# Kernel tuning notes

Hardware: AMD Instinct MI355X
Metric: run time of the kernel (lower is better)

Reference implementation:

```python
import jax, jax.numpy as jnp
import numpy as np

B, NQ, NKV = 16, 4096, 77
QUERY_DIM, CONTEXT_DIM = 320, 768
HEADS, DIM_HEAD = 8, 64
INNER = HEADS * DIM_HEAD
SCALE = DIM_HEAD ** (-0.5)
MAX_NEG = -jnp.finfo(jnp.float32).max / 2


def setup_inputs() -> dict:
    key = jax.random.key(0)
    ks = jax.random.split(key, 8)
    x = jax.random.normal(ks[0], (B, NQ, QUERY_DIM), dtype=jnp.float32)
    context = jax.random.normal(ks[1], (B, NKV, CONTEXT_DIM), dtype=jnp.float32)
    mask = jax.random.randint(ks[2], (B, 1, 1, NKV), 0, 2).astype(bool)
    s = 0.02
    Wq = jax.random.normal(ks[3], (QUERY_DIM, INNER), dtype=jnp.float32) * s
    Wk = jax.random.normal(ks[4], (CONTEXT_DIM, INNER), dtype=jnp.float32) * s
    Wv = jax.random.normal(ks[5], (CONTEXT_DIM, INNER), dtype=jnp.float32) * s
    Wo = jax.random.normal(ks[6], (INNER, QUERY_DIM), dtype=jnp.float32) * s
    bo = jnp.zeros((QUERY_DIM,), dtype=jnp.float32)
    return {"x": x, "context": context, "mask": mask,
            "Wq": Wq, "Wk": Wk, "Wv": Wv, "Wo": Wo, "bo": bo}


def reference(x, context, mask, Wq, Wk, Wv, Wo, bo):
    # projections (bias-free Linears)
    q = (x @ Wq).reshape(B, NQ, HEADS, DIM_HEAD)        # b q h d
    k = (context @ Wk).reshape(B, NKV, HEADS, DIM_HEAD)  # b k h d
    v = (context @ Wv).reshape(B, NKV, HEADS, DIM_HEAD)  # b k h d
    # additive mask bias: 0 where mask, -finfo.max/2 where ~mask (matches masked_fill_)
    bias = jnp.where(mask, jnp.float32(0), MAX_NEG)      # broadcast to b h q k
    sim = jnp.einsum('bqhd,bkhd->bhqk', q, k) * SCALE + bias
    attn = jax.nn.softmax(sim, axis=-1)
    out = jnp.einsum('bhqk,bkhd->bqhd', attn, v).reshape(B, NQ, INNER)
    return out @ Wo + bo  # dropout p=0 -> identity
```

## Files before the change

kernel.cpp:

```cpp
#include <hip/hip_runtime.h>

typedef unsigned short ushort_t;
typedef __attribute__((ext_vector_type(8))) short bf16x8;
typedef __attribute__((ext_vector_type(4))) float f32x4;

#define B_SZ   16
#define NQ     4096
#define NKV    77
#define QDIM   320
#define CDIM   768
#define HEADS  8
#define DHEAD  64
#define INNER  512
#define M_ROWS (B_SZ * NQ)
#define VT_STR 104

__device__ __forceinline__ ushort_t f2bf(float f) {
  unsigned u = __builtin_bit_cast(unsigned, f);
  u = (u + 0x7fffu + ((u >> 16) & 1u)) >> 16;
  return (ushort_t)u;
}

__device__ __forceinline__ void async16(const ushort_t* g, ushort_t* l) {
  __builtin_amdgcn_global_load_lds(
      (const __attribute__((address_space(1))) unsigned int*)g,
      (__attribute__((address_space(3))) unsigned int*)l,
      16, 0, 0);
}

#define VMCNT(N) asm volatile("s_waitcnt vmcnt(" #N ")" ::: "memory")

__global__ void mask_bias_kernel(const unsigned char* __restrict__ mraw,
                                 float* __restrict__ biasT) {
  __shared__ int s_u8, s_w4;
  if (threadIdx.x == 0) { s_u8 = 0; s_w4 = 0; }
  __syncthreads();
  const int nbytes = B_SZ * NKV;
  for (int i = threadIdx.x; i < nbytes; i += blockDim.x) {
    unsigned char v = mraw[i];
    if (v && (i & 3)) atomicOr(&s_u8, 1);
    if (v && ((i & 7) == 4)) atomicOr(&s_w4, 1);
  }
  __syncthreads();
  int mode = s_u8 ? 0 : (s_w4 ? 1 : 2);
  for (int i = threadIdx.x; i < B_SZ * 80; i += blockDim.x) {
    int b = i / 80, kv = i - b * 80;
    float bias = -2e30f;
    if (kv < NKV) {
      int idx = b * NKV + kv;
      long long m;
      if (mode == 0)      m = (long long)mraw[idx];
      else if (mode == 1) m = (long long)((const int*)mraw)[idx];
      else                m = ((const long long*)mraw)[idx];
      bias = m ? 0.0f : -1e30f;
    }
    biasT[i] = bias;
  }
}

__global__ void cast_f32_bf16(const float* __restrict__ in,
                              ushort_t* __restrict__ out, int n4) {
  int i = blockIdx.x * blockDim.x + threadIdx.x;
  int stride = gridDim.x * blockDim.x;
  const float4* in4 = (const float4*)in;
  ushort4* out4 = (ushort4*)out;
  for (; i < n4; i += stride) {
    float4 v = in4[i];
    ushort4 o;
    o.x = f2bf(v.x); o.y = f2bf(v.y); o.z = f2bf(v.z); o.w = f2bf(v.w);
    out4[i] = o;
  }
}

__global__ void tcast_f32_bf16(const float* __restrict__ in,
                               ushort_t* __restrict__ out,
                               int K, int N, int Npad, float scale) {
  int i = blockIdx.x * blockDim.x + threadIdx.x;
  int stride = gridDim.x * blockDim.x;
  int total = Npad * K;
  for (; i < total; i += stride) {
    int n = i / K, k = i - n * K;
    out[i] = (n < N) ? f2bf(in[(size_t)k * N + n] * scale) : (ushort_t)0;
  }
}

__global__ void vtrans_kernel(const ushort_t* __restrict__ kvb,
                              ushort_t* __restrict__ vt) {
  const int h = blockIdx.y, b = blockIdx.z;
  const int wid = threadIdx.x >> 6, lane = threadIdx.x & 63;
  const int d = blockIdx.x * 4 + wid;
  ushort_t* dst = vt + (size_t)(b * HEADS + h) * (64 * VT_STR) + d * VT_STR;
  for (int kv = lane; kv < VT_STR; kv += 64)
    dst[kv] = (kv < NKV)
        ? kvb[(size_t)(b * NKV + kv) * 1024 + 512 + h * 64 + d]
        : (ushort_t)0;
}

__global__ __launch_bounds__(256) void gemm_bf16(
    const ushort_t* __restrict__ A, const ushort_t* __restrict__ Bt,
    ushort_t* __restrict__ Cb,
    int K, int Astride, int Bstride, int Cstride) {
  __shared__ ushort_t As[128 * 64];
  __shared__ ushort_t Bs[128 * 64];
  const int tid = threadIdx.x;
  const int wid = tid >> 6, lane = tid & 63;
  const int wr = wid >> 1, wc = wid & 1;
  const int tileM = blockIdx.x * 128, tileN = blockIdx.y * 128;

  f32x4 acc[4][4];
#pragma unroll
  for (int m = 0; m < 4; ++m)
#pragma unroll
    for (int n = 0; n < 4; ++n) acc[m][n] = (f32x4){0.f, 0.f, 0.f, 0.f};

  const int srow = lane >> 3;
  const int scol = (lane & 7) * 8;

  for (int kt = 0; kt < K; kt += 64) {
    __syncthreads();
#pragma unroll
    for (int j = 0; j < 4; ++j) {
      int s = wid * 4 + j;
      const ushort_t* ga = A + (size_t)(tileM + s * 8 + srow) * Astride + kt + scol;
      const ushort_t* gb = Bt + (size_t)(tileN + s * 8 + srow) * Bstride + kt + scol;
      async16(ga, As + s * 512);
      async16(gb, Bs + s * 512);
    }
    __syncthreads();
#pragma unroll
    for (int kc = 0; kc < 2; ++kc) {
      bf16x8 af[4], bfr[4];
#pragma unroll
      for (int m = 0; m < 4; ++m)
        af[m] = *(const bf16x8*)&As[(wr * 64 + m * 16 + (lane & 15)) * 64 + kc * 32 + (lane >> 4) * 8];
#pragma unroll
      for (int n = 0; n < 4; ++n)
        bfr[n] = *(const bf16x8*)&Bs[(wc * 64 + n * 16 + (lane & 15)) * 64 + kc * 32 + (lane >> 4) * 8];
#pragma unroll
      for (int m = 0; m < 4; ++m)
#pragma unroll
        for (int n = 0; n < 4; ++n)
          acc[m][n] = __builtin_amdgcn_mfma_f32_16x16x32_bf16(af[m], bfr[n], acc[m][n], 0, 0, 0);
    }
  }

  const int r0 = tileM + wr * 64;
  const int c0 = tileN + wc * 64;
  const int rl2 = (lane >> 4) * 4;
  const int cl = lane & 15;
#pragma unroll
  for (int m = 0; m < 4; ++m)
#pragma unroll
    for (int n = 0; n < 4; ++n) {
      int col = c0 + n * 16 + cl;
#pragma unroll
      for (int r = 0; r < 4; ++r)
        Cb[(size_t)(r0 + m * 16 + rl2 + r) * Cstride + col] = f2bf(acc[m][n][r]);
    }
}

__global__ __launch_bounds__(512, 2) void gemm_qproj_p(
    const float* __restrict__ x, const ushort_t* __restrict__ Wt,
    ushort_t* __restrict__ qb) {
  extern __shared__ char sm[];
  const int tid = threadIdx.x, wid = tid >> 6, lane = tid & 63;
  const int rl = lane & 15, g = lane >> 4;
  const int wr = wid & 1, wc = wid >> 1;
  const size_t Mbase = (size_t)blockIdx.x * 128;

  size_t asrc[2]; unsigned adst[2];
#pragma unroll
  for (int i = 0; i < 2; ++i) {
    int c = tid + i * 512, row = c >> 3, c16 = c & 7;
    asrc[i] = (Mbase + row) * 1280 + (unsigned)((c16 * 16) ^ ((row & 7) << 4));
    adst[i] = c * 16;
  }
  size_t bsrc[4]; unsigned bdst[4];
#pragma unroll
  for (int i = 0; i < 4; ++i) {
    int c = tid + i * 512, row = c >> 2, c16 = c & 3;
    bsrc[i] = (size_t)row * 640 + (unsigned)((c16 * 16) ^ ((row & 3) << 4));
    bdst[i] = 16384 + c * 16;
  }
  const char* xB = (const char*)x;
  const char* WtB = (const char*)Wt;

  f32x4 acc[4][8];
#pragma unroll
  for (int m = 0; m < 4; ++m)
#pragma unroll
    for (int n = 0; n < 8; ++n) acc[m][n] = (f32x4){0.f, 0.f, 0.f, 0.f};

#define QSTAGE(K)                                                           \
  {                                                                         \
    char* bb = sm + (unsigned)((K) % 3) * 49152u;                           \
    _Pragma("unroll")                                                       \
    for (int i = 0; i < 2; ++i)                                             \
      async16((const ushort_t*)(xB + asrc[i] + (size_t)(K) * 128),          \
              (ushort_t*)(bb + adst[i]));                                   \
    _Pragma("unroll")                                                       \
    for (int i = 0; i < 4; ++i)                                             \
      async16((const ushort_t*)(WtB + bsrc[i] + (size_t)(K) * 64),          \
              (ushort_t*)(bb + bdst[i]));                                   \
  }

  QSTAGE(0)
  QSTAGE(1)
  for (int s = 0; s < 10; ++s) {
    if (s < 8) QSTAGE(s + 2)
    if (s < 8)       { VMCNT(12); }
    else if (s == 8) { VMCNT(6); }
    else             { VMCNT(0); }
    __builtin_amdgcn_sched_barrier(0);
    __builtin_amdgcn_s_barrier();
    __builtin_amdgcn_sched_barrier(0);

    const char* Ab = sm + (unsigned)(s % 3) * 49152u;
    const char* Bb = Ab + 16384;
    bf16x8 af[4], bfr[8];
#pragma unroll
    for (int m = 0; m < 4; ++m) {
      const int row = wr * 64 + m * 16 + rl;
      const int sw = (row & 7) << 4;
      f32x4 lo = *(const f32x4*)(Ab + row * 128 + ((g * 32) ^ sw));
      f32x4 hi = *(const f32x4*)(Ab + row * 128 + ((g * 32 + 16) ^ sw));
      unsigned w0, w1, w2, w3;
      asm("v_cvt_pk_bf16_f32 %0, %1, %2" : "=v"(w0) : "v"(lo[0]), "v"(lo[1]));
      asm("v_cvt_pk_bf16_f32 %0, %1, %2" : "=v"(w1) : "v"(lo[2]), "v"(lo[3]));
      asm("v_cvt_pk_bf16_f32 %0, %1, %2" : "=v"(w2) : "v"(hi[0]), "v"(hi[1]));
      asm("v_cvt_pk_bf16_f32 %0, %1, %2" : "=v"(w3) : "v"(hi[2]), "v"(hi[3]));
      union { unsigned u[4]; bf16x8 v; } cv;
      cv.u[0] = w0; cv.u[1] = w1; cv.u[2] = w2; cv.u[3] = w3;
      af[m] = cv.v;
    }
#pragma unroll
    for (int n = 0; n < 8; ++n) {
      const int row = wc * 128 + n * 16 + rl;
      bfr[n] = *(const bf16x8*)(Bb + row * 64 + ((g * 16) ^ ((row & 3) << 4)));
    }
#pragma unroll
    for (int m = 0; m < 4; ++m)
#pragma unroll
      for (int n = 0; n < 8; ++n)
        acc[m][n] = __builtin_amdgcn_mfma_f32_16x16x32_bf16(af[m], bfr[n], acc[m][n], 0, 0, 0);
    __builtin_amdgcn_sched_barrier(0);
    __builtin_amdgcn_s_barrier();
    __builtin_amdgcn_sched_barrier(0);
  }

  ushort_t* eb = (ushort_t*)sm;
#pragma unroll
  for (int h = 0; h < 2; ++h) {
    if (h) __syncthreads();
    if (wr == h) {
#pragma unroll
      for (int m = 0; m < 4; ++m)
#pragma unroll
        for (int n = 0; n < 8; ++n)
#pragma unroll
          for (int r = 0; r < 4; ++r)
            eb[(m * 16 + g * 4 + r) * 512 + wc * 128 + n * 16 + rl] = f2bf(acc[m][n][r]);
    }
    __syncthreads();
#pragma unroll
    for (int i = 0; i < 8; ++i) {
      int c = tid + i * 512, row = c >> 6;
      *(bf16x8*)(qb + (Mbase + h * 64 + row) * 512 + (c & 63) * 8) =
          *(const bf16x8*)(eb + c * 8);
    }
  }
}

__global__ __launch_bounds__(512, 2) void gemm_oproj_p(
    const ushort_t* __restrict__ A, const ushort_t* __restrict__ Wt,
    const float* __restrict__ bo, float* __restrict__ out) {
  extern __shared__ char sm[];
  const int tid = threadIdx.x, wid = tid >> 6, lane = tid & 63;
  const int rl = lane & 15, g = lane >> 4;
  const int wr = wid & 1, wc = wid >> 1;
  const size_t Mbase = (size_t)blockIdx.x * 128;

  size_t asrc; unsigned adst;
  {
    int c = tid, row = c >> 2, c16 = c & 3;
    asrc = (Mbase + row) * 1024 + (unsigned)((c16 * 16) ^ ((row & 3) << 4));
    adst = c * 16;
  }
  size_t bsrc[3]; unsigned bdst[3];
#pragma unroll
  for (int i = 0; i < 3; ++i) {
    int c = tid + i * 512, row = c >> 2, c16 = c & 3;
    bsrc[i] = (size_t)row * 1024 + (unsigned)((c16 * 16) ^ ((row & 3) << 4));
    bdst[i] = 8192 + c * 16;
  }
  const char* AB = (const char*)A;
  const char* WtB = (const char*)Wt;

  f32x4 acc[4][6];
#pragma unroll
  for (int m = 0; m < 4; ++m)
#pragma unroll
    for (int n = 0; n < 6; ++n) acc[m][n] = (f32x4){0.f, 0.f, 0.f, 0.f};

#define OSTAGE(K)                                                           \
  {                                                                         \
    char* bb = sm + (unsigned)((K) % 3) * 32768u;                           \
    async16((const ushort_t*)(AB + asrc + (size_t)(K) * 64),                \
            (ushort_t*)(bb + adst));                                        \
    _Pragma("unroll")                                                       \
    for (int i = 0; i < 3; ++i)                                             \
      async16((const ushort_t*)(WtB + bsrc[i] + (size_t)(K) * 64),          \
              (ushort_t*)(bb + bdst[i]));                                   \
  }

  OSTAGE(0)
  OSTAGE(1)
  for (int s = 0; s < 16; ++s) {
    if (s < 14) OSTAGE(s + 2)
    if (s < 14)       { VMCNT(8); }
    else if (s == 14) { VMCNT(4); }
    else              { VMCNT(0); }
    __builtin_amdgcn_sched_barrier(0);
    __builtin_amdgcn_s_barrier();
    __builtin_amdgcn_sched_barrier(0);

    const char* Ab = sm + (unsigned)(s % 3) * 32768u;
    const char* Bb = Ab + 8192;
    bf16x8 af[4], bfr[6];
#pragma unroll
    for (int m = 0; m < 4; ++m) {
      const int row = wr * 64 + m * 16 + rl;
      af[m] = *(const bf16x8*)(Ab + row * 64 + ((g * 16) ^ ((row & 3) << 4)));
    }
#pragma unroll
    for (int n = 0; n < 6; ++n) {
      const int row = wc * 96 + n * 16 + rl;
      bfr[n] = *(const bf16x8*)(Bb + row * 64 + ((g * 16) ^ ((row & 3) << 4)));
    }
#pragma unroll
    for (int m = 0; m < 4; ++m)
#pragma unroll
      for (int n = 0; n < 6; ++n)
        acc[m][n] = __builtin_amdgcn_mfma_f32_16x16x32_bf16(af[m], bfr[n], acc[m][n], 0, 0, 0);
    __builtin_amdgcn_sched_barrier(0);
    __builtin_amdgcn_s_barrier();
    __builtin_amdgcn_sched_barrier(0);
  }

  const size_t r0 = Mbase + wr * 64;
  const int c0 = wc * 96;
#pragma unroll
  for (int n = 0; n < 6; ++n) {
    int col = c0 + n * 16 + rl;
    if (col < QDIM) {
      float bv = bo[col];
#pragma unroll
      for (int m = 0; m < 4; ++m)
#pragma unroll
        for (int r = 0; r < 4; ++r)
          out[(r0 + m * 16 + g * 4 + r) * QDIM + col] = acc[m][n][r] + bv;
    }
  }
}

__global__ __launch_bounds__(256) void attn_kernel(
    const ushort_t* __restrict__ qb, const ushort_t* __restrict__ kvb,
    const ushort_t* __restrict__ vt, const float* __restrict__ biasT,
    ushort_t* __restrict__ ab) {
  __shared__ ushort_t Vt[64 * VT_STR];
  __shared__ ushort_t P[4 * 16 * VT_STR];
  const int qt = blockIdx.x, h = blockIdx.y, b = blockIdx.z;
  const int tid = threadIdx.x, wid = tid >> 6, lane = tid & 63;
  const int rl = lane & 15;
  const int kh = (lane >> 4) * 8;

  const ushort_t* vtg = vt + (size_t)(b * HEADS + h) * (64 * VT_STR);
  for (int i = tid; i < 832; i += 256) async16(vtg + i * 8, Vt + i * 8);
  for (int i = tid; i < 832; i += 256)
    *(bf16x8*)&P[i * 8] = (bf16x8){0, 0, 0, 0, 0, 0, 0, 0};

  bf16x8 kf[5][2];
  float bias_v[5];
#pragma unroll
  for (int nt = 0; nt < 5; ++nt) {
    int kv = nt * 16 + rl;
    bias_v[nt] = biasT[b * 80 + kv];
    kf[nt][0] = (bf16x8){0, 0, 0, 0, 0, 0, 0, 0};
    kf[nt][1] = (bf16x8){0, 0, 0, 0, 0, 0, 0, 0};
    if (kv < NKV) {
      const ushort_t* kp = &kvb[(size_t)(b * NKV + kv) * 1024 + h * 64 + kh];
      kf[nt][0] = *(const bf16x8*)kp;
      kf[nt][1] = *(const bf16x8*)(kp + 32);
    }
  }
  __syncthreads();

  const int qbase = b * NQ + qt * 256;
  const int pbase = wid * (16 * VT_STR);
#pragma unroll 1
  for (int chunk = 0; chunk < 4; ++chunk) {
    if (chunk) __syncthreads();
    const int row0 = chunk * 64 + wid * 16;

    const ushort_t* qp = &qb[(size_t)(qbase + row0 + rl) * INNER + h * 64 + kh];
    bf16x8 qf0 = *(const bf16x8*)qp;
    bf16x8 qf1 = *(const bf16x8*)(qp + 32);

    f32x4 s[5];
#pragma unroll
    for (int nt = 0; nt < 5; ++nt) {
      s[nt] = (f32x4){0.f, 0.f, 0.f, 0.f};
      s[nt] = __builtin_amdgcn_mfma_f32_16x16x32_bf16(qf0, kf[nt][0], s[nt], 0, 0, 0);
      s[nt] = __builtin_amdgcn_mfma_f32_16x16x32_bf16(qf1, kf[nt][1], s[nt], 0, 0, 0);
    }

    float mx[4] = {-3.0e38f, -3.0e38f, -3.0e38f, -3.0e38f};
#pragma unroll
    for (int nt = 0; nt < 5; ++nt)
#pragma unroll
      for (int r = 0; r < 4; ++r) {
        float v = s[nt][r] + bias_v[nt];
        s[nt][r] = v;
        mx[r] = fmaxf(mx[r], v);
      }
#pragma unroll
    for (int d = 1; d < 16; d <<= 1)
#pragma unroll
      for (int r = 0; r < 4; ++r) mx[r] = fmaxf(mx[r], __shfl_xor(mx[r], d, 64));

    float sm_[4] = {0.f, 0.f, 0.f, 0.f};
#pragma unroll
    for (int nt = 0; nt < 5; ++nt)
#pragma unroll
      for (int r = 0; r < 4; ++r) {
        float p = __expf(s[nt][r] - mx[r]);
        s[nt][r] = p;
        sm_[r] += p;
      }
#pragma unroll
    for (int d = 1; d < 16; d <<= 1)
#pragma unroll
      for (int r = 0; r < 4; ++r) sm_[r] += __shfl_xor(sm_[r], d, 64);

    float rcp[4];
#pragma unroll
    for (int r = 0; r < 4; ++r) rcp[r] = 1.0f / sm_[r];

#pragma unroll
    for (int nt = 0; nt < 5; ++nt)
#pragma unroll
      for (int r = 0; r < 4; ++r)
        P[pbase + ((lane >> 4) * 4 + r) * VT_STR + nt * 16 + rl] = f2bf(s[nt][r]);

    f32x4 o[4];
#pragma unroll
    for (int n = 0; n < 4; ++n) o[n] = (f32x4){0.f, 0.f, 0.f, 0.f};
#pragma unroll
    for (int kc = 0; kc < 3; ++kc) {
      bf16x8 pf = *(const bf16x8*)&P[pbase + rl * VT_STR + kc * 32 + kh];
#pragma unroll
      for (int n = 0; n < 4; ++n) {
        bf16x8 vf = *(const bf16x8*)&Vt[(n * 16 + rl) * VT_STR + kc * 32 + kh];
        o[n] = __builtin_amdgcn_mfma_f32_16x16x32_bf16(pf, vf, o[n], 0, 0, 0);
      }
    }

#pragma unroll
    for (int n = 0; n < 4; ++n)
#pragma unroll
      for (int r = 0; r < 4; ++r)
        P[pbase + ((lane >> 4) * 4 + r) * VT_STR + n * 16 + rl] = f2bf(o[n][r] * rcp[r]);

    __syncthreads();

    {
      const int rflat = tid >> 2, d0 = (tid & 3) * 16;
      const ushort_t* src = &P[(rflat >> 4) * (16 * VT_STR) + (rflat & 15) * VT_STR + d0];
      ushort_t* dst = &ab[(size_t)(qbase + chunk * 64 + rflat) * INNER + h * 64 + d0];
      *(bf16x8*)dst = *(const bf16x8*)src;
      *(bf16x8*)(dst + 8) = *(const bf16x8*)(src + 8);
    }
  }
}

extern "C" void kernel_launch(void* const* d_in, const int* in_sizes, int n_in,
                              void* d_out, int out_size, void* d_ws, size_t ws_size,
                              hipStream_t stream) {
  (void)in_sizes; (void)n_in; (void)out_size; (void)ws_size;
  const float* x   = (const float*)d_in[0];
  const float* ctx = (const float*)d_in[1];
  const unsigned char* mask = (const unsigned char*)d_in[2];
  const float* Wq = (const float*)d_in[3];
  const float* Wk = (const float*)d_in[4];
  const float* Wv = (const float*)d_in[5];
  const float* Wo = (const float*)d_in[6];
  const float* bo = (const float*)d_in[7];
  float* out = (float*)d_out;

  hipFuncSetAttribute((const void*)gemm_qproj_p,
                      hipFuncAttributeMaxDynamicSharedMemorySize, 147456);
  hipFuncSetAttribute((const void*)gemm_oproj_p,
                      hipFuncAttributeMaxDynamicSharedMemorySize, 98304);

  char* ws = (char*)d_ws;
  size_t off = 0;
  auto alloc = [&](size_t bytes) {
    char* p = ws + off;
    off += (bytes + 255) & ~(size_t)255;
    return p;
  };
  float*    biasT = (float*)alloc(B_SZ * 80 * sizeof(float));
  ushort_t* ab    = (ushort_t*)alloc((size_t)M_ROWS * INNER * 2);
  ushort_t* qb    = (ushort_t*)alloc((size_t)M_ROWS * INNER * 2);
  ushort_t* cb    = (ushort_t*)alloc((size_t)1280 * CDIM * 2);
  ushort_t* Wqb   = (ushort_t*)alloc((size_t)INNER * QDIM * 2);
  ushort_t* Wkvb  = (ushort_t*)alloc((size_t)1024 * CDIM * 2);
  ushort_t* Wob   = (ushort_t*)alloc((size_t)384 * INNER * 2);
  ushort_t* kvb   = (ushort_t*)alloc((size_t)1280 * 1024 * 2);
  ushort_t* vt    = (ushort_t*)alloc((size_t)B_SZ * HEADS * 64 * VT_STR * 2);

  mask_bias_kernel<<<1, 256, 0, stream>>>(mask, biasT);
  cast_f32_bf16<<<512, 256, 0, stream>>>(ctx, cb, B_SZ * NKV * CDIM / 4);
  tcast_f32_bf16<<<640, 256, 0, stream>>>(Wq, Wqb, QDIM, INNER, INNER, 0.125f);
  tcast_f32_bf16<<<1536, 256, 0, stream>>>(Wk, Wkvb, CDIM, INNER, INNER, 1.0f);
  tcast_f32_bf16<<<1536, 256, 0, stream>>>(Wv, Wkvb + (size_t)INNER * CDIM, CDIM, INNER, INNER, 1.0f);
  tcast_f32_bf16<<<768, 256, 0, stream>>>(Wo, Wob, INNER, QDIM, 384, 1.0f);

  gemm_qproj_p<<<M_ROWS / 128, 512, 147456, stream>>>(x, Wqb, qb);
  dim3 g2(1280 / 128, 1024 / 128);
  gemm_bf16<<<g2, 256, 0, stream>>>(cb, Wkvb, kvb, CDIM, CDIM, CDIM, 1024);
  vtrans_kernel<<<dim3(16, HEADS, B_SZ), 256, 0, stream>>>(kvb, vt);
  attn_kernel<<<dim3(NQ / 256, HEADS, B_SZ), 256, 0, stream>>>(qb, kvb, vt, biasT, ab);
  gemm_oproj_p<<<M_ROWS / 128, 512, 98304, stream>>>(ab, Wob, bo, out);
}
```

Baseline: 190.8 us.

## Restructure Q projection into small 32-row tiles with full-K LDS staging

Replaces the 128-row pipelined, triple-buffered Q-projection GEMM with a kernel that handles 32 rows per block. Each block converts its full 32x320 x tile to bf16 once into swizzled LDS, and each wave reads its weight fragments straight from global memory instead of staging them. The aim is to cut LDS footprint and raise occupancy (launch bounds 4 blocks) while spreading work over four times as many blocks. In exchange the weights are re-read from global or L2 by every block, there is no async pipelining, and the outputs are written with scattered 2-byte stores instead of the staged coalesced write.

```diff
diff --git a/kernel.cpp b/kernel.cpp
--- a/kernel.cpp
+++ b/kernel.cpp
@@ -26,6 +26,17 @@
       (const __attribute__((address_space(1))) unsigned int*)g,
       (__attribute__((address_space(3))) unsigned int*)l,
       16, 0, 0);
+}
+
+__device__ __forceinline__ bf16x8 cvt8(f32x4 lo, f32x4 hi) {
+  unsigned w0, w1, w2, w3;
+  asm("v_cvt_pk_bf16_f32 %0, %1, %2" : "=v"(w0) : "v"(lo[0]), "v"(lo[1]));
+  asm("v_cvt_pk_bf16_f32 %0, %1, %2" : "=v"(w1) : "v"(lo[2]), "v"(lo[3]));
+  asm("v_cvt_pk_bf16_f32 %0, %1, %2" : "=v"(w2) : "v"(hi[0]), "v"(hi[1]));
+  asm("v_cvt_pk_bf16_f32 %0, %1, %2" : "=v"(w3) : "v"(hi[2]), "v"(hi[3]));
+  union { unsigned u[4]; bf16x8 v; } cv;
+  cv.u[0] = w0; cv.u[1] = w1; cv.u[2] = w2; cv.u[3] = w3;
+  return cv.v;
 }
 
 #define VMCNT(N) asm volatile("s_waitcnt vmcnt(" #N ")" ::: "memory")
@@ -159,116 +170,55 @@
     }
 }
 
-__global__ __launch_bounds__(512, 2) void gemm_qproj_p(
+__global__ __launch_bounds__(512, 4) void gemm_qproj_r9(
     const float* __restrict__ x, const ushort_t* __restrict__ Wt,
     ushort_t* __restrict__ qb) {
-  extern __shared__ char sm[];
+  __shared__ ushort_t As[32 * 320];
   const int tid = threadIdx.x, wid = tid >> 6, lane = tid & 63;
   const int rl = lane & 15, g = lane >> 4;
-  const int wr = wid & 1, wc = wid >> 1;
-  const size_t Mbase = (size_t)blockIdx.x * 128;
-
-  size_t asrc[2]; unsigned adst[2];
-#pragma unroll
-  for (int i = 0; i < 2; ++i) {
-    int c = tid + i * 512, row = c >> 3, c16 = c & 7;
-    asrc[i] = (Mbase + row) * 1280 + (unsigned)((c16 * 16) ^ ((row & 7) << 4));
-    adst[i] = c * 16;
-  }
-  size_t bsrc[4]; unsigned bdst[4];
-#pragma unroll
-  for (int i = 0; i < 4; ++i) {
-    int c = tid + i * 512, row = c >> 2, c16 = c & 3;
-    bsrc[i] = (size_t)row * 640 + (unsigned)((c16 * 16) ^ ((row & 3) << 4));
-    bdst[i] = 16384 + c * 16;
-  }
-  const char* xB = (const char*)x;
-  const char* WtB = (const char*)Wt;
-
-  f32x4 acc[4][8];
-#pragma unroll
-  for (int m = 0; m < 4; ++m)
-#pragma unroll
-    for (int n = 0; n < 8; ++n) acc[m][n] = (f32x4){0.f, 0.f, 0.f, 0.f};
-
-#define QSTAGE(K)                                                           \
-  {                                                                         \
-    char* bb = sm + (unsigned)((K) % 3) * 49152u;                           \
-    _Pragma("unroll")                                                       \
-    for (int i = 0; i < 2; ++i)                                             \
-      async16((const ushort_t*)(xB + asrc[i] + (size_t)(K) * 128),          \
-              (ushort_t*)(bb + adst[i]));                                   \
-    _Pragma("unroll")                                                       \
-    for (int i = 0; i < 4; ++i)                                             \
-      async16((const ushort_t*)(WtB + bsrc[i] + (size_t)(K) * 64),          \
-              (ushort_t*)(bb + bdst[i]));                                   \
-  }
-
-  QSTAGE(0)
-  QSTAGE(1)
-  for (int s = 0; s < 10; ++s) {
-    if (s < 8) QSTAGE(s + 2)
-    if (s < 8)       { VMCNT(12); }
-    else if (s == 8) { VMCNT(6); }
-    else             { VMCNT(0); }
-    __builtin_amdgcn_sched_barrier(0);
-    __builtin_amdgcn_s_barrier();
-    __builtin_amdgcn_sched_barrier(0);
-
-    const char* Ab = sm + (unsigned)(s % 3) * 49152u;
-    const char* Bb = Ab + 16384;
-    bf16x8 af[4], bfr[8];
-#pragma unroll
-    for (int m = 0; m < 4; ++m) {
-      const int row = wr * 64 + m * 16 + rl;
-      const int sw = (row & 7) << 4;
-      f32x4 lo = *(const f32x4*)(Ab + row * 128 + ((g * 32) ^ sw));
-      f32x4 hi = *(const f32x4*)(Ab + row * 128 + ((g * 32 + 16) ^ sw));
-      unsigned w0, w1, w2, w3;
-      asm("v_cvt_pk_bf16_f32 %0, %1, %2" : "=v"(w0) : "v"(lo[0]), "v"(lo[1]));
-      asm("v_cvt_pk_bf16_f32 %0, %1, %2" : "=v"(w1) : "v"(lo[2]), "v"(lo[3]));
-      asm("v_cvt_pk_bf16_f32 %0, %1, %2" : "=v"(w2) : "v"(hi[0]), "v"(hi[1]));
-      asm("v_cvt_pk_bf16_f32 %0, %1, %2" : "=v"(w3) : "v"(hi[2]), "v"(hi[3]));
-      union { unsigned u[4]; bf16x8 v; } cv;
-      cv.u[0] = w0; cv.u[1] = w1; cv.u[2] = w2; cv.u[3] = w3;
-      af[m] = cv.v;
-    }
-#pragma unroll
-    for (int n = 0; n < 8; ++n) {
-      const int row = wc * 128 + n * 16 + rl;
-      bfr[n] = *(const bf16x8*)(Bb + row * 64 + ((g * 16) ^ ((row & 3) << 4)));
-    }
-#pragma unroll
-    for (int m = 0; m < 4; ++m)
-#pragma unroll
-      for (int n = 0; n < 8; ++n)
+  const size_t Mbase = (size_t)blockIdx.x * 32;
+
+  for (int c = tid; c < 1280; c += 512) {
+    int row = c / 40, c16 = c - row * 40;
+    const f32x4* src = (const f32x4*)&x[(Mbase + row) * 320 + c16 * 8];
+    *(bf16x8*)&As[row * 320 + ((c16 ^ (row & 7)) << 3)] = cvt8(src[0], src[1]);
+  }
+  __syncthreads();
+
+  f32x4 acc[2][4];
+#pragma unroll
+  for (int m = 0; m < 2; ++m)
+#pragma unroll
+    for (int n = 0; n < 4; ++n) acc[m][n] = (f32x4){0.f, 0.f, 0.f, 0.f};
+
+#pragma unroll
+  for (int kc = 0; kc < 10; ++kc) {
+    bf16x8 bfr[4];
+#pragma unroll
+    for (int n = 0; n < 4; ++n)
+      bfr[n] = *(const bf16x8*)&Wt[(size_t)(wid * 64 + n * 16 + rl) * QDIM + kc * 32 + g * 8];
+    bf16x8 af[2];
+#pragma unroll
+    for (int m = 0; m < 2; ++m) {
+      const int row = m * 16 + rl;
+      af[m] = *(const bf16x8*)&As[row * 320 + (((kc * 4 + g) ^ (row & 7)) << 3)];
+    }
+#pragma unroll
+    for (int m = 0; m < 2; ++m)
+#pragma unroll
+      for (int n = 0; n < 4; ++n)
         acc[m][n] = __builtin_amdgcn_mfma_f32_16x16x32_bf16(af[m], bfr[n], acc[m][n], 0, 0, 0);
-    __builtin_amdgcn_sched_barrier(0);
-    __builtin_amdgcn_s_barrier();
-    __builtin_amdgcn_sched_barrier(0);
-  }
-
-  ushort_t* eb = (ushort_t*)sm;
-#pragma unroll
-  for (int h = 0; h < 2; ++h) {
-    if (h) __syncthreads();
-    if (wr == h) {
-#pragma unroll
-      for (int m = 0; m < 4; ++m)
-#pragma unroll
-        for (int n = 0; n < 8; ++n)
-#pragma unroll
-          for (int r = 0; r < 4; ++r)
-            eb[(m * 16 + g * 4 + r) * 512 + wc * 128 + n * 16 + rl] = f2bf(acc[m][n][r]);
-    }
-    __syncthreads();
-#pragma unroll
-    for (int i = 0; i < 8; ++i) {
-      int c = tid + i * 512, row = c >> 6;
-      *(bf16x8*)(qb + (Mbase + h * 64 + row) * 512 + (c & 63) * 8) =
-          *(const bf16x8*)(eb + c * 8);
-    }
-  }
+  }
+
+#pragma unroll
+  for (int m = 0; m < 2; ++m)
+#pragma unroll
+    for (int n = 0; n < 4; ++n) {
+      const int col = wid * 64 + n * 16 + rl;
+#pragma unroll
+      for (int r = 0; r < 4; ++r)
+        qb[(Mbase + m * 16 + g * 4 + r) * INNER + col] = f2bf(acc[m][n][r]);
+    }
 }
 
 __global__ __launch_bounds__(512, 2) void gemm_oproj_p(
@@ -497,8 +447,6 @@
   const float* bo = (const float*)d_in[7];
   float* out = (float*)d_out;
 
-  hipFuncSetAttribute((const void*)gemm_qproj_p,
-                      hipFuncAttributeMaxDynamicSharedMemorySize, 147456);
   hipFuncSetAttribute((const void*)gemm_oproj_p,
                       hipFuncAttributeMaxDynamicSharedMemorySize, 98304);
 
@@ -526,7 +474,7 @@
   tcast_f32_bf16<<<1536, 256, 0, stream>>>(Wv, Wkvb + (size_t)INNER * CDIM, CDIM, INNER, INNER, 1.0f);
   tcast_f32_bf16<<<768, 256, 0, stream>>>(Wo, Wob, INNER, QDIM, 384, 1.0f);
 
-  gemm_qproj_p<<<M_ROWS / 128, 512, 147456, stream>>>(x, Wqb, qb);
+  gemm_qproj_r9<<<M_ROWS / 32, 512, 0, stream>>>(x, Wqb, qb);
   dim3 g2(1280 / 128, 1024 / 128);
   gemm_bf16<<<g2, 256, 0, stream>>>(cb, Wkvb, kvb, CDIM, CDIM, CDIM, 1024);
   vtrans_kernel<<<dim3(16, HEADS, B_SZ), 256, 0, stream>>>(kvb, vt);
```

After: 237.6 us. 24.6% more time.
